# Performance work log

Hardware: AMD Instinct MI355X
Metric: run time of the kernel (lower is better)

## Reference

```python
import jax, jax.numpy as jnp
import numpy as np


def setup_inputs() -> dict:
    key = jax.random.key(0)
    x = jax.random.normal(key, (4, 3, 8192), dtype=jnp.float32)  # (B, 3, N)
    return {"x": x, "k": 30}


def reference(x, k):
    # x: (B, 3, N)
    x_t = jnp.swapaxes(x, 1, 2)  # (B, N, 3)
    xx = jnp.sum(x_t ** 2, axis=2, keepdims=True)  # (B, N, 1)
    # pairwise squared distances (B, N, N)
    pairwise = xx + jnp.swapaxes(xx, 1, 2) - 2.0 * jnp.matmul(x_t, x)
    # k smallest distances -> negate and take top_k
    _, idx = jax.lax.top_k(-pairwise, k)  # idx: (B, N, k)
    # gather neighbors: (B, N, k, 3)
    neighbors = jax.vmap(lambda pts, i: pts[i])(x_t, idx)
    centroid = jnp.mean(neighbors, axis=2, keepdims=True)  # (B, N, 1, 3)
    centered = neighbors - centroid  # (B, N, k, 3)
    # per-point 3x3 covariance
    cov = jnp.einsum('bnki,bnkj->bnij', centered, centered)  # (B, N, 3, 3)
    _, v = jnp.linalg.eigh(cov)  # eigenvalues ascending
    normals = v[..., :, 0]  # eigenvector of smallest eigenvalue, (B, N, 3)
    # orient normals toward viewpoint (origin): view_dir = -x_t
    dot = jnp.sum(-x_t * normals, axis=-1, keepdims=True)
    normals = jnp.where(dot < 0, -normals, normals)
    x_out = jnp.concatenate([x, jnp.swapaxes(normals, 1, 2)], axis=1)  # (B, 6, N)
    return x_out
```

## Files before the change

### kernel.cpp

```cpp
#include <hip/hip_runtime.h>
#include <math.h>

#define N_PTS   8192
#define KNN     30
#define CAPG    104
#define STR     105
#define GROUPS  8
#define BLOCK   128
#define NZ      64
#define NY      64
#define NBKT    (NZ * NY)
#define CLO     -4.0f
#define CSC     8.0f
#define INVCSC  0.125f
#define LAMBDA  40.0f
#define RBINS   2048
#define RWMAX   32.0f
#define RSCALE  ((float)RBINS / RWMAX)


__device__ __forceinline__ int clampi(int v, int lo, int hi) {
    return v < lo ? lo : (v > hi ? hi : v);
}
__device__ __forceinline__ int bucket_of(float pz, float py) {
    int zb = clampi((int)floorf((pz - CLO) * CSC), 0, NZ - 1);
    int yb = clampi((int)floorf((py - CLO) * CSC), 0, NY - 1);
    return (zb << 6) | yb;
}

__global__ __launch_bounds__(1024) void prep_kernel(const float* __restrict__ x,
                                                    float4* __restrict__ S,
                                                    int* __restrict__ O,
                                                    int* __restrict__ bstart,
                                                    float* __restrict__ R2T,
                                                    float* __restrict__ out) {
    __shared__ int hist[NBKT];
    __shared__ int cur[NBKT];
    __shared__ int wsum[16];

    const int b = blockIdx.x;
    const int t = threadIdx.x;
    const int wid = t >> 6, lane = t & 63;
    const float* xb = x + (size_t)b * 3 * N_PTS;
    float* ob = out + (size_t)b * 6 * N_PTS;

    for (int k = t; k < NBKT; k += 1024) hist[k] = 0;
    __syncthreads();

    float px[8], py[8], pz[8];
    int   bk[8];
    #pragma unroll
    for (int u = 0; u < 8; ++u) {
        int i = (u << 10) + t;
        px[u] = xb[i]; py[u] = xb[N_PTS + i]; pz[u] = xb[2 * N_PTS + i];
        bk[u] = bucket_of(pz[u], py[u]);
        atomicAdd(&hist[bk[u]], 1);
        ob[i]             = px[u];
        ob[N_PTS + i]     = py[u];
        ob[2 * N_PTS + i] = pz[u];
    }
    __syncthreads();

    int l0 = hist[4 * t], l1 = hist[4 * t + 1], l2 = hist[4 * t + 2], l3 = hist[4 * t + 3];
    int s = l0 + l1 + l2 + l3;
    int sum = s;
    #pragma unroll
    for (int off = 1; off < 64; off <<= 1) {
        int v = __shfl_up(sum, off);
        if (lane >= off) sum += v;
    }
    if (lane == 63) wsum[wid] = sum;
    __syncthreads();
    if (t == 0) {
        int run = 0;
        #pragma unroll
        for (int k = 0; k < 16; ++k) { int v = wsum[k]; wsum[k] = run; run += v; }
    }
    __syncthreads();
    int base = wsum[wid] + (sum - s);
    int b0 = base, b1 = base + l0, b2 = b1 + l1, b3 = b2 + l2;
    cur[4 * t] = b0; cur[4 * t + 1] = b1; cur[4 * t + 2] = b2; cur[4 * t + 3] = b3;
    int* bsb = bstart + b * (NBKT + 1);
    bsb[4 * t] = b0; bsb[4 * t + 1] = b1; bsb[4 * t + 2] = b2; bsb[4 * t + 3] = b3;
    if (t == 1023) bsb[NBKT] = N_PTS;
    __syncthreads();

    float4* Sb = S + ((size_t)b << 13);
    int*    Ob = O + ((size_t)b << 13);
    #pragma unroll
    for (int u = 0; u < 8; ++u) {
        int dst = atomicAdd(&cur[bk[u]], 1);
        float xx = __fadd_rn(__fadd_rn(__fmul_rn(px[u], px[u]), __fmul_rn(py[u], py[u])),
                             __fmul_rn(pz[u], pz[u]));
        Sb[dst] = make_float4(px[u], py[u], pz[u], xx);
        Ob[dst] = (u << 10) + t;
    }

    if (b == 0) {
        for (int k = t; k < RBINS; k += 1024) {
            float wrep = ((float)k + 0.5f) * (RWMAX / (float)RBINS);
            float c = fmaxf(sqrtf(wrep), 1e-3f);
            float rlo = 0.05f, rhi = 6.0f;
            for (int it = 0; it < 20; ++it) {
                float r = 0.5f * (rlo + rhi);
                float slo = fmaxf(c - r, 0.0f);
                float h = (c + r - slo) * 0.125f;
                float f = 0.0f;
                #pragma unroll
                for (int l = 0; l <= 8; ++l) {
                    float sq = slo + h * (float)l;
                    float cs = c - sq;
                    float hh = fmaxf(fminf((r * r - cs * cs) * (0.5f / c), 2.0f * sq), 0.0f);
                    float wq = (l == 0 || l == 8) ? 1.0f : ((l & 1) ? 4.0f : 2.0f);
                    f += wq * __expf(-0.5f * sq * sq) * sq * hh;
                }
                float lam = 1089.3f * f * h;
                if (lam < LAMBDA) rlo = r; else rhi = r;
            }
            float rad = rhi * 1.02f;
            R2T[k] = rad * rad;
        }
    }
}

__global__ __launch_bounds__(BLOCK, 6) void knn_normal_kernel(const float4* __restrict__ S,
                                                              const int* __restrict__ O,
                                                              const int* __restrict__ bstart,
                                                              const float* __restrict__ R2T,
                                                              float* __restrict__ out) {
    __shared__ unsigned long long ldk[GROUPS * STR];

    const int t    = threadIdx.x;
    const int l16  = t & 15;
    const int g    = t >> 4;
    const int gsh  = (t & 63) & ~15;
    const int qblk = (blockIdx.x * 1031) & 4095;
    const int qid  = qblk * GROUPS + g;
    const int b    = qid >> 13;
    const int pos  = qid & (N_PTS - 1);
    const float4* __restrict__ P  = S + ((size_t)b << 13);
    const int*    __restrict__ Ob = O + ((size_t)b << 13);
    const int*    __restrict__ bs = bstart + b * (NBKT + 1);
    const float4 qp = P[pos];
    const int    oi = Ob[pos];

    unsigned long long* __restrict__ ldg = ldk + g * STR;

    const int rbin = min((int)(qp.w * RSCALE), RBINS - 1);
    float r2 = R2T[rbin];

    int  cnt = 0;
    bool active = true;

    for (;;) {
        if (active) {
            cnt = 0;
            float w  = __fmaf_rn(sqrtf(r2), 1.002f, 1e-3f);
            float w2 = __fmul_rn(w, w);
            int zlo = clampi((int)floorf((qp.z - w - CLO) * CSC), 0, NZ - 1);
            int zhi = clampi((int)floorf((qp.z + w - CLO) * CSC), 0, NZ - 1);
            for (int zb = zlo; zb <= zhi; ++zb) {
                float z0  = CLO + (float)zb * INVCSC;
                float dzr = fmaxf(fmaxf(z0 - qp.z, qp.z - (z0 + INVCSC)), 0.0f) * 0.999f;
                float hw2 = __fmaf_rn(-dzr, dzr, w2);
                if (hw2 <= 0.0f) continue;
                float hw  = __fmaf_rn(sqrtf(hw2), 1.001f, 1e-4f);
                int ylo = clampi((int)floorf((qp.y - hw - CLO) * CSC), 0, NY - 1);
                int yhi = clampi((int)floorf((qp.y + hw - CLO) * CSC), 0, NY - 1);
                int lo = bs[(zb << 6) + ylo];
                int hi = bs[(zb << 6) + yhi + 1];
                int smax = (hi - lo + 31) >> 5;
                for (int s = 0; s < smax; ++s) {
                    int j1  = lo + (s << 5) + l16;
                    int j2  = j1 + 16;
                    int jc1 = j1 < hi ? j1 : hi - 1;
                    int jc2 = j2 < hi ? j2 : hi - 1;
                    float4 p1 = P[jc1];
                    float4 p2 = P[jc2];
                    float mm1 = __fmaf_rn(qp.z, p1.z, __fmaf_rn(qp.y, p1.y, __fmul_rn(qp.x, p1.x)));
                    float d1  = __fsub_rn(__fadd_rn(qp.w, p1.w), __fmul_rn(2.0f, mm1));
                    float mm2 = __fmaf_rn(qp.z, p2.z, __fmaf_rn(qp.y, p2.y, __fmul_rn(qp.x, p2.x)));
                    float d2  = __fsub_rn(__fadd_rn(qp.w, p2.w), __fmul_rn(2.0f, mm2));
                    bool hit1 = (j1 < hi) && (d1 <= r2);
                    bool hit2 = (j2 < hi) && (d2 <= r2);
                    unsigned long long m1 = __ballot(hit1);
                    unsigned sub1 = (unsigned)((m1 >> gsh) & 0xFFFFull);
                    if (hit1) {
                        int slot = cnt + __popc(sub1 & ((1u << l16) - 1u));
                        if (slot < CAPG) {
                            unsigned u = __float_as_uint(d1);
                            u = (u & 0x80000000u) ? ~u : (u | 0x80000000u);
                            ldg[slot] = ((unsigned long long)u << 28) | (unsigned long long)jc1;
                        }
                    }
                    cnt += __popc(sub1);
                    unsigned long long m2 = __ballot(hit2);
                    unsigned sub2 = (unsigned)((m2 >> gsh) & 0xFFFFull);
                    if (hit2) {
                        int slot = cnt + __popc(sub2 & ((1u << l16) - 1u));
                        if (slot < CAPG) {
                            unsigned u = __float_as_uint(d2);
                            u = (u & 0x80000000u) ? ~u : (u | 0x80000000u);
                            ldg[slot] = ((unsigned long long)u << 28) | (unsigned long long)jc2;
                        }
                    }
                    cnt += __popc(sub2);
                }
            }
        }
        bool bad = active && (cnt < KNN || cnt > CAPG);
        if (__ballot(bad) == 0ULL) break;
        active = bad;
        if (active) r2 = (cnt < KNN) ? r2 * 1.6f : r2 * 0.82f;
    }

    for (int k = l16; k < cnt; k += 16) {
        unsigned long long key = ldg[k];
        int jc = (int)(key & 0x3FFFull);
        ldg[k] = (key & ~0x0FFFFFFFull) | ((unsigned long long)Ob[jc] << 14) | (unsigned long long)jc;
    }
    __syncthreads();

    const double qx = (double)qp.x, qy = (double)qp.y, qz = (double)qp.z;
    double sx = 0.0, sy = 0.0, sz = 0.0;
    double sxx = 0.0, sxy = 0.0, sxz = 0.0, syy = 0.0, syz = 0.0, szz = 0.0;

    for (int k = l16; k < cnt; k += 16) {
        unsigned long long key = ldg[k];
        int rank = 0;
        for (int u = 0; u < cnt; ++u) rank += (ldg[u] < key) ? 1 : 0;
        if (rank < KNN) {
            float4 p = P[(int)(key & 0x3FFFull)];
            double ax = (double)p.x - qx, ay = (double)p.y - qy, az = (double)p.z - qz;
            sx += ax; sy += ay; sz += az;
            sxx = fma(ax, ax, sxx); sxy = fma(ax, ay, sxy); sxz = fma(ax, az, sxz);
            syy = fma(ay, ay, syy); syz = fma(ay, az, syz); szz = fma(az, az, szz);
        }
    }

    #pragma unroll
    for (int off = 1; off < 16; off <<= 1) {
        sx  += __shfl_xor(sx,  off, 16); sy  += __shfl_xor(sy,  off, 16); sz  += __shfl_xor(sz,  off, 16);
        sxx += __shfl_xor(sxx, off, 16); sxy += __shfl_xor(sxy, off, 16); sxz += __shfl_xor(sxz, off, 16);
        syy += __shfl_xor(syy, off, 16); syz += __shfl_xor(syz, off, 16); szz += __shfl_xor(szz, off, 16);
    }

    if (l16 == 0) {
        const double kinv = 1.0 / (double)KNN;
        double m00 = sxx - sx * sx * kinv;
        double m11 = syy - sy * sy * kinv;
        double m22 = szz - sz * sz * kinv;
        double m01 = sxy - sx * sy * kinv;
        double m02 = sxz - sx * sz * kinv;
        double m12 = syz - sy * sz * kinv;

        double nx = 1.0, ny = 0.0, nz = 0.0;
        double q3 = (m00 + m11 + m22) / 3.0;
        double p1 = m01 * m01 + m02 * m02 + m12 * m12;
        double d00 = m00 - q3, d11 = m11 - q3, d22 = m22 - q3;
        double p2 = d00 * d00 + d11 * d11 + d22 * d22 + 2.0 * p1;
        if (p2 > 1e-280) {
            double pp = sqrt(p2 / 6.0);
            double ip = 1.0 / pp;
            double b00 = d00 * ip, b11 = d11 * ip, b22 = d22 * ip;
            double b01 = m01 * ip, b02 = m02 * ip, b12 = m12 * ip;
            double detB = b00 * (b11 * b22 - b12 * b12)
                        - b01 * (b01 * b22 - b12 * b02)
                        + b02 * (b01 * b12 - b11 * b02);
            double rr = 0.5 * detB;
            rr = rr < -1.0 ? -1.0 : (rr > 1.0 ? 1.0 : rr);
            double phi = acos(rr) / 3.0;
            double lam = q3 + 2.0 * pp * cos(phi + 2.0943951023931953);
            double a00 = m00 - lam, a11 = m11 - lam, a22 = m22 - lam;
            double v0x = m01 * m12 - m02 * a11, v0y = m02 * m01 - a00 * m12, v0z = a00 * a11 - m01 * m01;
            double v1x = m01 * a22 - m02 * m12, v1y = m02 * m02 - a00 * a22, v1z = a00 * m12 - m01 * m02;
            double v2x = a11 * a22 - m12 * m12, v2y = m12 * m02 - m01 * a22, v2z = m01 * m12 - a11 * m02;
            double n0 = v0x * v0x + v0y * v0y + v0z * v0z;
            double n1 = v1x * v1x + v1y * v1y + v1z * v1z;
            double n2 = v2x * v2x + v2y * v2y + v2z * v2z;
            double bx = v0x, by = v0y, bz = v0z, bn = n0;
            if (n1 > bn) { bx = v1x; by = v1y; bz = v1z; bn = n1; }
            if (n2 > bn) { bx = v2x; by = v2y; bz = v2z; bn = n2; }
            if (bn > 1e-280) {
                double inv = 1.0 / sqrt(bn);
                nx = bx * inv; ny = by * inv; nz = bz * inv;
            }
        }
        double dq = -(qx * nx + qy * ny + qz * nz);
        if (dq < 0.0) { nx = -nx; ny = -ny; nz = -nz; }

        float* ob = out + (size_t)b * 6 * N_PTS;
        ob[3 * N_PTS + oi] = (float)nx;
        ob[4 * N_PTS + oi] = (float)ny;
        ob[5 * N_PTS + oi] = (float)nz;
    }
}

extern "C" void kernel_launch(void* const* d_in, const int* in_sizes, int n_in,
                              void* d_out, int out_size, void* d_ws, size_t ws_size,
                              hipStream_t stream) {
    const float* x = (const float*)d_in[0];
    float* out = (float*)d_out;
    char* ws = (char*)d_ws;
    float4* S    = (float4*)(ws);
    int*    O    = (int*)(ws + 524288);
    int*    bsta = (int*)(ws + 655360);
    float*  r2t  = (float*)(ws + 720912);

    prep_kernel<<<dim3(4), dim3(1024), 0, stream>>>(x, S, O, bsta, r2t, out);
    knn_normal_kernel<<<dim3(32768 / GROUPS), dim3(BLOCK), 0, stream>>>(S, O, bsta, r2t, out);
}
```

Measured before the change: 184.9 us.

## Scan each query's grid cells with a full wavefront and move radius table to own block

The candidate-gathering loop used to give each query a 16-lane group. It now walks the four queries of a wavefront one after another, with all 64 lanes scanning 128 candidates per step for each query, and the rank/covariance phases stay per-group. Wave-level barriers replace the block-wide syncthreads. The radius lookup-table bisection moves from block 0 of the prep kernel into a dedicated fifth block, so it no longer serializes behind one batch's bucketing. The aim is better lane use when bucket ranges are short or uneven and less divergence between queries, at the cost of running the four queries' searches serially.

```diff
diff --git a/kernel.cpp b/kernel.cpp
--- a/kernel.cpp
+++ b/kernel.cpp
@@ -40,63 +40,8 @@
 
     const int b = blockIdx.x;
     const int t = threadIdx.x;
-    const int wid = t >> 6, lane = t & 63;
-    const float* xb = x + (size_t)b * 3 * N_PTS;
-    float* ob = out + (size_t)b * 6 * N_PTS;
-
-    for (int k = t; k < NBKT; k += 1024) hist[k] = 0;
-    __syncthreads();
-
-    float px[8], py[8], pz[8];
-    int   bk[8];
-    #pragma unroll
-    for (int u = 0; u < 8; ++u) {
-        int i = (u << 10) + t;
-        px[u] = xb[i]; py[u] = xb[N_PTS + i]; pz[u] = xb[2 * N_PTS + i];
-        bk[u] = bucket_of(pz[u], py[u]);
-        atomicAdd(&hist[bk[u]], 1);
-        ob[i]             = px[u];
-        ob[N_PTS + i]     = py[u];
-        ob[2 * N_PTS + i] = pz[u];
-    }
-    __syncthreads();
-
-    int l0 = hist[4 * t], l1 = hist[4 * t + 1], l2 = hist[4 * t + 2], l3 = hist[4 * t + 3];
-    int s = l0 + l1 + l2 + l3;
-    int sum = s;
-    #pragma unroll
-    for (int off = 1; off < 64; off <<= 1) {
-        int v = __shfl_up(sum, off);
-        if (lane >= off) sum += v;
-    }
-    if (lane == 63) wsum[wid] = sum;
-    __syncthreads();
-    if (t == 0) {
-        int run = 0;
-        #pragma unroll
-        for (int k = 0; k < 16; ++k) { int v = wsum[k]; wsum[k] = run; run += v; }
-    }
-    __syncthreads();
-    int base = wsum[wid] + (sum - s);
-    int b0 = base, b1 = base + l0, b2 = b1 + l1, b3 = b2 + l2;
-    cur[4 * t] = b0; cur[4 * t + 1] = b1; cur[4 * t + 2] = b2; cur[4 * t + 3] = b3;
-    int* bsb = bstart + b * (NBKT + 1);
-    bsb[4 * t] = b0; bsb[4 * t + 1] = b1; bsb[4 * t + 2] = b2; bsb[4 * t + 3] = b3;
-    if (t == 1023) bsb[NBKT] = N_PTS;
-    __syncthreads();
-
-    float4* Sb = S + ((size_t)b << 13);
-    int*    Ob = O + ((size_t)b << 13);
-    #pragma unroll
-    for (int u = 0; u < 8; ++u) {
-        int dst = atomicAdd(&cur[bk[u]], 1);
-        float xx = __fadd_rn(__fadd_rn(__fmul_rn(px[u], px[u]), __fmul_rn(py[u], py[u])),
-                             __fmul_rn(pz[u], pz[u]));
-        Sb[dst] = make_float4(px[u], py[u], pz[u], xx);
-        Ob[dst] = (u << 10) + t;
-    }
-
-    if (b == 0) {
+
+    if (b == 4) {
         for (int k = t; k < RBINS; k += 1024) {
             float wrep = ((float)k + 0.5f) * (RWMAX / (float)RBINS);
             float c = fmaxf(sqrtf(wrep), 1e-3f);
@@ -120,6 +65,63 @@
             float rad = rhi * 1.02f;
             R2T[k] = rad * rad;
         }
+        return;
+    }
+
+    const int wid = t >> 6, lane = t & 63;
+    const float* xb = x + (size_t)b * 3 * N_PTS;
+    float* ob = out + (size_t)b * 6 * N_PTS;
+
+    for (int k = t; k < NBKT; k += 1024) hist[k] = 0;
+    __syncthreads();
+
+    float px[8], py[8], pz[8];
+    int   bk[8];
+    #pragma unroll
+    for (int u = 0; u < 8; ++u) {
+        int i = (u << 10) + t;
+        px[u] = xb[i]; py[u] = xb[N_PTS + i]; pz[u] = xb[2 * N_PTS + i];
+        bk[u] = bucket_of(pz[u], py[u]);
+        atomicAdd(&hist[bk[u]], 1);
+        ob[i]             = px[u];
+        ob[N_PTS + i]     = py[u];
+        ob[2 * N_PTS + i] = pz[u];
+    }
+    __syncthreads();
+
+    int l0 = hist[4 * t], l1 = hist[4 * t + 1], l2 = hist[4 * t + 2], l3 = hist[4 * t + 3];
+    int s = l0 + l1 + l2 + l3;
+    int sum = s;
+    #pragma unroll
+    for (int off = 1; off < 64; off <<= 1) {
+        int v = __shfl_up(sum, off);
+        if (lane >= off) sum += v;
+    }
+    if (lane == 63) wsum[wid] = sum;
+    __syncthreads();
+    if (t == 0) {
+        int run = 0;
+        #pragma unroll
+        for (int k = 0; k < 16; ++k) { int v = wsum[k]; wsum[k] = run; run += v; }
+    }
+    __syncthreads();
+    int base = wsum[wid] + (sum - s);
+    int b0 = base, b1 = base + l0, b2 = b1 + l1, b3 = b2 + l2;
+    cur[4 * t] = b0; cur[4 * t + 1] = b1; cur[4 * t + 2] = b2; cur[4 * t + 3] = b3;
+    int* bsb = bstart + b * (NBKT + 1);
+    bsb[4 * t] = b0; bsb[4 * t + 1] = b1; bsb[4 * t + 2] = b2; bsb[4 * t + 3] = b3;
+    if (t == 1023) bsb[NBKT] = N_PTS;
+    __syncthreads();
+
+    float4* Sb = S + ((size_t)b << 13);
+    int*    Ob = O + ((size_t)b << 13);
+    #pragma unroll
+    for (int u = 0; u < 8; ++u) {
+        int dst = atomicAdd(&cur[bk[u]], 1);
+        float xx = __fadd_rn(__fadd_rn(__fmul_rn(px[u], px[u]), __fmul_rn(py[u], py[u])),
+                             __fmul_rn(pz[u], pz[u]));
+        Sb[dst] = make_float4(px[u], py[u], pz[u], xx);
+        Ob[dst] = (u << 10) + t;
     }
 }
 
@@ -131,95 +133,104 @@
     __shared__ unsigned long long ldk[GROUPS * STR];
 
     const int t    = threadIdx.x;
+    const int lane = t & 63;
+    const int wv   = t >> 6;
     const int l16  = t & 15;
     const int g    = t >> 4;
-    const int gsh  = (t & 63) & ~15;
+    const int gw   = g & 3;
     const int qblk = (blockIdx.x * 1031) & 4095;
     const int qid  = qblk * GROUPS + g;
     const int b    = qid >> 13;
     const int pos  = qid & (N_PTS - 1);
     const float4* __restrict__ P  = S + ((size_t)b << 13);
     const int*    __restrict__ Ob = O + ((size_t)b << 13);
-    const int*    __restrict__ bs = bstart + b * (NBKT + 1);
     const float4 qp = P[pos];
     const int    oi = Ob[pos];
 
     unsigned long long* __restrict__ ldg = ldk + g * STR;
 
-    const int rbin = min((int)(qp.w * RSCALE), RBINS - 1);
-    float r2 = R2T[rbin];
-
-    int  cnt = 0;
-    bool active = true;
-
-    for (;;) {
-        if (active) {
+    int cnts[4];
+    #pragma unroll
+    for (int sub = 0; sub < 4; ++sub) {
+        const int qs_id  = qblk * GROUPS + (wv << 2) + sub;
+        const int bs_    = qs_id >> 13;
+        const int pos_s  = qs_id & (N_PTS - 1);
+        const float4* __restrict__ Ps  = S + ((size_t)bs_ << 13);
+        const int*    __restrict__ bss = bstart + bs_ * (NBKT + 1);
+        const float4 qs = Ps[pos_s];
+        const int rb = min((int)(qs.w * RSCALE), RBINS - 1);
+        float r2s = R2T[rb];
+        unsigned long long* __restrict__ row = ldk + ((wv << 2) + sub) * STR;
+
+        int cnt;
+        for (;;) {
             cnt = 0;
-            float w  = __fmaf_rn(sqrtf(r2), 1.002f, 1e-3f);
+            float w  = __fmaf_rn(sqrtf(r2s), 1.002f, 1e-3f);
             float w2 = __fmul_rn(w, w);
-            int zlo = clampi((int)floorf((qp.z - w - CLO) * CSC), 0, NZ - 1);
-            int zhi = clampi((int)floorf((qp.z + w - CLO) * CSC), 0, NZ - 1);
+            int zlo = clampi((int)floorf((qs.z - w - CLO) * CSC), 0, NZ - 1);
+            int zhi = clampi((int)floorf((qs.z + w - CLO) * CSC), 0, NZ - 1);
             for (int zb = zlo; zb <= zhi; ++zb) {
                 float z0  = CLO + (float)zb * INVCSC;
-                float dzr = fmaxf(fmaxf(z0 - qp.z, qp.z - (z0 + INVCSC)), 0.0f) * 0.999f;
+                float dzr = fmaxf(fmaxf(z0 - qs.z, qs.z - (z0 + INVCSC)), 0.0f) * 0.999f;
                 float hw2 = __fmaf_rn(-dzr, dzr, w2);
                 if (hw2 <= 0.0f) continue;
                 float hw  = __fmaf_rn(sqrtf(hw2), 1.001f, 1e-4f);
-                int ylo = clampi((int)floorf((qp.y - hw - CLO) * CSC), 0, NY - 1);
-                int yhi = clampi((int)floorf((qp.y + hw - CLO) * CSC), 0, NY - 1);
-                int lo = bs[(zb << 6) + ylo];
-                int hi = bs[(zb << 6) + yhi + 1];
-                int smax = (hi - lo + 31) >> 5;
+                int ylo = clampi((int)floorf((qs.y - hw - CLO) * CSC), 0, NY - 1);
+                int yhi = clampi((int)floorf((qs.y + hw - CLO) * CSC), 0, NY - 1);
+                int lo = bss[(zb << 6) + ylo];
+                int hi = bss[(zb << 6) + yhi + 1];
+                int smax = (hi - lo + 127) >> 7;
                 for (int s = 0; s < smax; ++s) {
-                    int j1  = lo + (s << 5) + l16;
-                    int j2  = j1 + 16;
+                    int j1  = lo + (s << 7) + lane;
+                    int j2  = j1 + 64;
                     int jc1 = j1 < hi ? j1 : hi - 1;
                     int jc2 = j2 < hi ? j2 : hi - 1;
-                    float4 p1 = P[jc1];
-                    float4 p2 = P[jc2];
-                    float mm1 = __fmaf_rn(qp.z, p1.z, __fmaf_rn(qp.y, p1.y, __fmul_rn(qp.x, p1.x)));
-                    float d1  = __fsub_rn(__fadd_rn(qp.w, p1.w), __fmul_rn(2.0f, mm1));
-                    float mm2 = __fmaf_rn(qp.z, p2.z, __fmaf_rn(qp.y, p2.y, __fmul_rn(qp.x, p2.x)));
-                    float d2  = __fsub_rn(__fadd_rn(qp.w, p2.w), __fmul_rn(2.0f, mm2));
-                    bool hit1 = (j1 < hi) && (d1 <= r2);
-                    bool hit2 = (j2 < hi) && (d2 <= r2);
+                    float4 p1 = Ps[jc1];
+                    float4 p2 = Ps[jc2];
+                    float mm1 = __fmaf_rn(qs.z, p1.z, __fmaf_rn(qs.y, p1.y, __fmul_rn(qs.x, p1.x)));
+                    float d1  = __fsub_rn(__fadd_rn(qs.w, p1.w), __fmul_rn(2.0f, mm1));
+                    float mm2 = __fmaf_rn(qs.z, p2.z, __fmaf_rn(qs.y, p2.y, __fmul_rn(qs.x, p2.x)));
+                    float d2  = __fsub_rn(__fadd_rn(qs.w, p2.w), __fmul_rn(2.0f, mm2));
+                    bool hit1 = (j1 < hi) && (d1 <= r2s);
+                    bool hit2 = (j2 < hi) && (d2 <= r2s);
                     unsigned long long m1 = __ballot(hit1);
-                    unsigned sub1 = (unsigned)((m1 >> gsh) & 0xFFFFull);
                     if (hit1) {
-                        int slot = cnt + __popc(sub1 & ((1u << l16) - 1u));
+                        int slot = cnt + __popcll(m1 & ((1ull << lane) - 1ull));
                         if (slot < CAPG) {
                             unsigned u = __float_as_uint(d1);
                             u = (u & 0x80000000u) ? ~u : (u | 0x80000000u);
-                            ldg[slot] = ((unsigned long long)u << 28) | (unsigned long long)jc1;
+                            row[slot] = ((unsigned long long)u << 28) | (unsigned long long)jc1;
                         }
                     }
-                    cnt += __popc(sub1);
+                    cnt += __popcll(m1);
                     unsigned long long m2 = __ballot(hit2);
-                    unsigned sub2 = (unsigned)((m2 >> gsh) & 0xFFFFull);
                     if (hit2) {
-                        int slot = cnt + __popc(sub2 & ((1u << l16) - 1u));
+                        int slot = cnt + __popcll(m2 & ((1ull << lane) - 1ull));
                         if (slot < CAPG) {
                             unsigned u = __float_as_uint(d2);
                             u = (u & 0x80000000u) ? ~u : (u | 0x80000000u);
-                            ldg[slot] = ((unsigned long long)u << 28) | (unsigned long long)jc2;
+                            row[slot] = ((unsigned long long)u << 28) | (unsigned long long)jc2;
                         }
                     }
-                    cnt += __popc(sub2);
+                    cnt += __popcll(m2);
                 }
             }
+            if (cnt >= KNN && cnt <= CAPG) break;
+            r2s = (cnt < KNN) ? r2s * 1.6f : r2s * 0.82f;
         }
-        bool bad = active && (cnt < KNN || cnt > CAPG);
-        if (__ballot(bad) == 0ULL) break;
-        active = bad;
-        if (active) r2 = (cnt < KNN) ? r2 * 1.6f : r2 * 0.82f;
-    }
+        cnts[sub] = cnt;
+    }
+    const int cnt = (gw == 0) ? cnts[0] : (gw == 1) ? cnts[1] : (gw == 2) ? cnts[2] : cnts[3];
+    __builtin_amdgcn_wave_barrier();
+    asm volatile("s_waitcnt lgkmcnt(0)" ::: "memory");
 
     for (int k = l16; k < cnt; k += 16) {
         unsigned long long key = ldg[k];
         int jc = (int)(key & 0x3FFFull);
         ldg[k] = (key & ~0x0FFFFFFFull) | ((unsigned long long)Ob[jc] << 14) | (unsigned long long)jc;
     }
-    __syncthreads();
+    __builtin_amdgcn_wave_barrier();
+    asm volatile("s_waitcnt lgkmcnt(0)" ::: "memory");
 
     const double qx = (double)qp.x, qy = (double)qp.y, qz = (double)qp.z;
     double sx = 0.0, sy = 0.0, sz = 0.0;
@@ -307,6 +318,6 @@
     int*    bsta = (int*)(ws + 655360);
     float*  r2t  = (float*)(ws + 720912);
 
-    prep_kernel<<<dim3(4), dim3(1024), 0, stream>>>(x, S, O, bsta, r2t, out);
+    prep_kernel<<<dim3(5), dim3(1024), 0, stream>>>(x, S, O, bsta, r2t, out);
     knn_normal_kernel<<<dim3(32768 / GROUPS), dim3(BLOCK), 0, stream>>>(S, O, bsta, r2t, out);
 }
```

After: 200.2 us. 1.08x slower.
